# Kernel tuning notes

Measured on AMD Instinct MI355X. Metric: run time of the kernel, lower is better.

Reference implementation:

```python
import jax, jax.numpy as jnp
import numpy as np

EPS = 1e-8

def setup_inputs() -> dict:
    key = jax.random.key(0)
    ks = jax.random.split(key, 4)
    B, N, D = 16, 2048, 1024
    APP = 1024
    x = jax.random.normal(ks[0], (B, N, D), dtype=jnp.float32)
    mask = jax.random.uniform(ks[1], (N, B), dtype=jnp.float32)  # [N, B] per original
    Wp = jax.random.normal(ks[2], (1024, D), dtype=jnp.float32) * 0.02
    bp = jnp.zeros((1024,), dtype=jnp.float32)
    Wv = jax.random.normal(ks[3], (APP, D), dtype=jnp.float32) * 0.02
    bv = jnp.zeros((APP,), dtype=jnp.float32)
    return {"x": x, "mask": mask, "Wp": Wp, "bp": bp, "Wv": Wv, "bv": bv}

def reference(x, mask, Wp, bp, Wv, bv):
    # proj + ReLU: [B,N,1024]
    xp = jax.nn.relu(jnp.einsum('bnd,pd->bnp', x, Wp) + bp)
    # L2-normalize along feature dim (matches xp / (norm + eps))
    xp = xp / (jnp.linalg.norm(xp, axis=2, keepdims=True) + EPS)
    # mask: [N,B] -> [B,N] (transpose+reshape in original yields [B,1,N])
    m = mask.T  # [B, N]
    # att_i = sum_j m_j * <xp_i, xp_j> / sum_j m_j  == <xp_i, sum_j m_j xp_j> / sum_j m_j
    ws = jnp.einsum('bn,bnp->bp', m, xp)                # [B, 1024]
    att = jnp.einsum('bnp,bp->bn', xp, ws) / jnp.sum(m, axis=1, keepdims=True)  # [B, N]
    # value + ReLU: [B,N,APP]
    xv = jax.nn.relu(jnp.einsum('bnd,ad->bna', x, Wv) + bv)
    return att[:, :, None] * xv
```

## Files before the change

kernel.cpp:

```cpp
#include <hip/hip_runtime.h>

#define B_  16
#define N_  2048
#define D_  1024
#define P_  1024
#define M_  (B_*N_)

typedef __attribute__((ext_vector_type(8))) short bf16x8;
typedef __attribute__((ext_vector_type(4))) float f32x4;

__device__ __forceinline__ float bf2f(unsigned short u) {
    union { unsigned int i; float f; } v; v.i = ((unsigned int)u) << 16; return v.f;
}
__device__ __forceinline__ unsigned short f2bf(float f) {
    union { unsigned int i; float f; } v; v.f = f;
    unsigned int i = v.i;
    return (unsigned short)((i + 0x7FFFu + ((i >> 16) & 1u)) >> 16);
}

__device__ __forceinline__ void async_cp16(const void* g, void* s) {
    __builtin_amdgcn_global_load_lds((const __attribute__((address_space(1))) void*)g,
                                     (__attribute__((address_space(3))) void*)s,
                                     16, 0, 0);
}

__global__ void cvt_k(const float* __restrict__ in, unsigned short* __restrict__ out, int n)
{
    for (int i = (blockIdx.x * 256 + threadIdx.x) * 4; i < n; i += gridDim.x * 256 * 4) {
        float4 v = *(const float4*)(in + i);
        union { unsigned short u[4]; unsigned long long ll; } p;
        p.u[0] = f2bf(v.x); p.u[1] = f2bf(v.y); p.u[2] = f2bf(v.z); p.u[3] = f2bf(v.w);
        *(unsigned long long*)(out + i) = p.ll;
    }
}

template<int MODE>
__global__ __launch_bounds__(256) void gemm_bf(const unsigned short* __restrict__ A,
                                               const unsigned short* __restrict__ W,
                                               const float* __restrict__ bias,
                                               const float* __restrict__ att,
                                               void* __restrict__ Cv)
{
    const int K = D_, BK = 32;
    __shared__ unsigned short As[128 * 32];
    __shared__ unsigned short Bs[128 * 32];

    const int wave = threadIdx.x >> 6, lane = threadIdx.x & 63;
    const int wr = wave >> 1, wc = wave & 1;
    const int m0 = blockIdx.y * 128, p0 = blockIdx.x * 128;

    const int srow = wave * 32 + (lane >> 2);
    const int scol = (lane & 3) * 8;
    const unsigned short* ag = A + (size_t)(m0 + srow) * K + scol;
    const unsigned short* bg = W + (size_t)(p0 + srow) * K + scol;
    unsigned short* as = &As[srow * BK + scol];
    unsigned short* bs = &Bs[srow * BK + scol];

    f32x4 acc[4][4];
    #pragma unroll
    for (int i = 0; i < 4; i++)
        #pragma unroll
        for (int j = 0; j < 4; j++) acc[i][j] = (f32x4){0.f,0.f,0.f,0.f};

    const int lr = lane & 15, lq = lane >> 4;
    const unsigned short* Ar = &As[(wr * 64 + lr) * BK + lq * 8];
    const unsigned short* Br = &Bs[(wc * 64 + lr) * BK + lq * 8];

    for (int kb = 0; kb < K; kb += BK) {
        async_cp16(ag + kb,          as);
        async_cp16(ag + 16 * K + kb, as + 16 * BK);
        async_cp16(bg + kb,          bs);
        async_cp16(bg + 16 * K + kb, bs + 16 * BK);
        __syncthreads();
        bf16x8 af[4], bf[4];
        #pragma unroll
        for (int i = 0; i < 4; i++) af[i] = *(const bf16x8*)(Ar + i * 16 * BK);
        #pragma unroll
        for (int j = 0; j < 4; j++) bf[j] = *(const bf16x8*)(Br + j * 16 * BK);
        #pragma unroll
        for (int i = 0; i < 4; i++)
            #pragma unroll
            for (int j = 0; j < 4; j++)
                acc[i][j] = __builtin_amdgcn_mfma_f32_16x16x32_bf16(af[i], bf[j], acc[i][j], 0, 0, 0);
        __syncthreads();
    }

    const int crow0 = m0 + wr * 64 + lq * 4;
    const int ccol0 = p0 + wc * 64 + lr;
    #pragma unroll
    for (int i = 0; i < 4; i++) {
        float attv[4];
        if (MODE == 1) {
            #pragma unroll
            for (int v = 0; v < 4; v++) attv[v] = att[crow0 + i * 16 + v];
        }
        #pragma unroll
        for (int j = 0; j < 4; j++) {
            const int col = ccol0 + j * 16;
            const float bi = bias[col];
            #pragma unroll
            for (int v = 0; v < 4; v++) {
                const int row = crow0 + i * 16 + v;
                float val = fmaxf(acc[i][j][v] + bi, 0.0f);
                if (MODE == 0) ((unsigned short*)Cv)[(size_t)row * P_ + col] = f2bf(val);
                else           ((float*)Cv)[(size_t)row * P_ + col] = val * attv[v];
            }
        }
    }
}

template<int MODE>
__global__ __launch_bounds__(256) void gemm_f32(const float* __restrict__ A,
                                                const float* __restrict__ W,
                                                const float* __restrict__ bias,
                                                const float* __restrict__ att,
                                                void* __restrict__ Cv)
{
    const int K = D_, BK = 32;
    __shared__ float As[128 * 32];
    __shared__ float Bs[128 * 32];

    const int wave = threadIdx.x >> 6, lane = threadIdx.x & 63;
    const int wr = wave >> 1, wc = wave & 1;
    const int m0 = blockIdx.y * 128, p0 = blockIdx.x * 128;

    const int srow = wave * 32 + (lane >> 3);
    const int scol = (lane & 7) * 4;
    const float* ag = A + (size_t)(m0 + srow) * K + scol;
    const float* bg = W + (size_t)(p0 + srow) * K + scol;
    float* as = &As[srow * BK + scol];
    float* bs = &Bs[srow * BK + scol];

    f32x4 acc[4][4];
    #pragma unroll
    for (int i = 0; i < 4; i++)
        #pragma unroll
        for (int j = 0; j < 4; j++) acc[i][j] = (f32x4){0.f,0.f,0.f,0.f};

    const int lr = lane & 15, lq = lane >> 4;
    const float* Ar = &As[(wr * 64 + lr) * BK + lq * 8];
    const float* Br = &Bs[(wc * 64 + lr) * BK + lq * 8];

    for (int kb = 0; kb < K; kb += BK) {
        #pragma unroll
        for (int s = 0; s < 4; s++) {
            async_cp16(ag + (size_t)s * 8 * K + kb, as + s * 8 * BK);
            async_cp16(bg + (size_t)s * 8 * K + kb, bs + s * 8 * BK);
        }
        __syncthreads();
        bf16x8 af[4], bf[4];
        #pragma unroll
        for (int i = 0; i < 4; i++) {
            f32x4 a0 = *(const f32x4*)(Ar + i * 16 * BK);
            f32x4 a1 = *(const f32x4*)(Ar + i * 16 * BK + 4);
            #pragma unroll
            for (int e = 0; e < 4; e++) {
                union { float f; unsigned int u; } c;
                c.f = a0[e]; af[i][e]     = (short)(c.u >> 16);
                c.f = a1[e]; af[i][e + 4] = (short)(c.u >> 16);
            }
        }
        #pragma unroll
        for (int j = 0; j < 4; j++) {
            f32x4 b0 = *(const f32x4*)(Br + j * 16 * BK);
            f32x4 b1 = *(const f32x4*)(Br + j * 16 * BK + 4);
            #pragma unroll
            for (int e = 0; e < 4; e++) {
                union { float f; unsigned int u; } c;
                c.f = b0[e]; bf[j][e]     = (short)(c.u >> 16);
                c.f = b1[e]; bf[j][e + 4] = (short)(c.u >> 16);
            }
        }
        #pragma unroll
        for (int i = 0; i < 4; i++)
            #pragma unroll
            for (int j = 0; j < 4; j++)
                acc[i][j] = __builtin_amdgcn_mfma_f32_16x16x32_bf16(af[i], bf[j], acc[i][j], 0, 0, 0);
        __syncthreads();
    }

    const int crow0 = m0 + wr * 64 + lq * 4;
    const int ccol0 = p0 + wc * 64 + lr;
    #pragma unroll
    for (int i = 0; i < 4; i++) {
        float attv[4];
        if (MODE == 1) {
            #pragma unroll
            for (int v = 0; v < 4; v++) attv[v] = att[crow0 + i * 16 + v];
        }
        #pragma unroll
        for (int j = 0; j < 4; j++) {
            const int col = ccol0 + j * 16;
            const float bi = bias[col];
            #pragma unroll
            for (int v = 0; v < 4; v++) {
                const int row = crow0 + i * 16 + v;
                float val = fmaxf(acc[i][j][v] + bi, 0.0f);
                if (MODE == 0) ((unsigned short*)Cv)[(size_t)row * P_ + col] = f2bf(val);
                else           ((float*)Cv)[(size_t)row * P_ + col] = val * attv[v];
            }
        }
    }
}

__global__ void rownorm_k(const unsigned short* __restrict__ X1,
                          const float* __restrict__ mask,
                          float* __restrict__ inv, float* __restrict__ wgt)
{
    const int r = blockIdx.x * 4 + (threadIdx.x >> 6);
    const int lane = threadIdx.x & 63;
    const unsigned short* row = X1 + (size_t)r * P_;
    bf16x8 u0 = *(const bf16x8*)(row + lane * 8);
    bf16x8 u1 = *(const bf16x8*)(row + 512 + lane * 8);
    float s = 0.f;
    #pragma unroll
    for (int k = 0; k < 8; k++) { float a = bf2f((unsigned short)u0[k]); s += a * a; }
    #pragma unroll
    for (int k = 0; k < 8; k++) { float a = bf2f((unsigned short)u1[k]); s += a * a; }
    #pragma unroll
    for (int off = 32; off > 0; off >>= 1) s += __shfl_down(s, off);
    if (lane == 0) {
        float iv = 1.f / (sqrtf(s) + 1e-8f);
        int b = r >> 11, n = r & (N_ - 1);
        inv[r] = iv;
        wgt[r] = mask[n * B_ + b] * iv;
    }
}

__global__ void msum_k(const float* __restrict__ mask, float* __restrict__ msum)
{
    const int b = blockIdx.x;
    float s = 0.f;
    for (int n = threadIdx.x; n < N_; n += 256) s += mask[n * B_ + b];
    __shared__ float red[256];
    red[threadIdx.x] = s; __syncthreads();
    for (int o = 128; o > 0; o >>= 1) {
        if (threadIdx.x < o) red[threadIdx.x] += red[threadIdx.x + o];
        __syncthreads();
    }
    if (threadIdx.x == 0) msum[b] = red[0];
}

__global__ void colreduce_k(const unsigned short* __restrict__ X1,
                            const float* __restrict__ wgt,
                            float* __restrict__ wsvec)
{
    const int b  = blockIdx.y;
    const int nc = blockIdx.x;
    const int p4 = threadIdx.x * 4;
    float s0 = 0, s1 = 0, s2 = 0, s3 = 0;
    const int rbase = b * N_ + nc * 128;
    for (int n = 0; n < 128; n++) {
        const int r = rbase + n;
        const float w = wgt[r];
        unsigned long long d = *(const unsigned long long*)(X1 + (size_t)r * P_ + p4);
        s0 += w * bf2f((unsigned short)(d));
        s1 += w * bf2f((unsigned short)(d >> 16));
        s2 += w * bf2f((unsigned short)(d >> 32));
        s3 += w * bf2f((unsigned short)(d >> 48));
    }
    float* dst = wsvec + b * P_ + p4;
    atomicAdd(dst + 0, s0); atomicAdd(dst + 1, s1);
    atomicAdd(dst + 2, s2); atomicAdd(dst + 3, s3);
}

__global__ void att_k(const unsigned short* __restrict__ X1,
                      const float* __restrict__ wsvec,
                      const float* __restrict__ inv,
                      const float* __restrict__ msum,
                      float* __restrict__ att)
{
    const int r = blockIdx.x * 4 + (threadIdx.x >> 6);
    const int lane = threadIdx.x & 63;
    const int b = r >> 11;
    const unsigned short* row = X1 + (size_t)r * P_;
    const float* w = wsvec + b * P_;
    bf16x8 u0 = *(const bf16x8*)(row + lane * 8);
    bf16x8 u1 = *(const bf16x8*)(row + 512 + lane * 8);
    float s = 0.f;
    #pragma unroll
    for (int k = 0; k < 8; k++) s += bf2f((unsigned short)u0[k]) * w[lane * 8 + k];
    #pragma unroll
    for (int k = 0; k < 8; k++) s += bf2f((unsigned short)u1[k]) * w[512 + lane * 8 + k];
    #pragma unroll
    for (int off = 32; off > 0; off >>= 1) s += __shfl_down(s, off);
    if (lane == 0) att[r] = s * inv[r] / msum[b];
}

extern "C" void kernel_launch(void* const* d_in, const int* in_sizes, int n_in,
                              void* d_out, int out_size, void* d_ws, size_t ws_size,
                              hipStream_t stream)
{
    const float* x    = (const float*)d_in[0];
    const float* mask = (const float*)d_in[1];
    const float* Wp   = (const float*)d_in[2];
    const float* bp   = (const float*)d_in[3];
    const float* Wv   = (const float*)d_in[4];
    const float* bv   = (const float*)d_in[5];
    float* out = (float*)d_out;

    unsigned short* X1 = (unsigned short*)d_out;

    const size_t xb_bytes = (size_t)M_ * D_ * 2;
    const size_t wb_bytes = (size_t)P_ * D_ * 2;
    const size_t f_bytes  = 3 * (size_t)M_ * 4 + (size_t)B_ * P_ * 4 + 64;
    const bool big_ws = ws_size >= xb_bytes + 2 * wb_bytes + f_bytes;

    char* ws = (char*)d_ws;
    size_t off = 0;
    unsigned short *xb = nullptr, *Wpb = nullptr, *Wvb = nullptr;
    if (big_ws) {
        xb  = (unsigned short*)(ws + off); off += xb_bytes;
        Wpb = (unsigned short*)(ws + off); off += wb_bytes;
        Wvb = (unsigned short*)(ws + off); off += wb_bytes;
    }
    float* inv  = (float*)(ws + off); off += (size_t)M_ * 4;
    float* wgt  = (float*)(ws + off); off += (size_t)M_ * 4;
    float* att  = (float*)(ws + off); off += (size_t)M_ * 4;
    float* wsv  = (float*)(ws + off); off += (size_t)B_ * P_ * 4;
    float* msum = (float*)(ws + off); off += 64;

    hipMemsetAsync(wsv, 0, (size_t)B_ * P_ * 4, stream);

    dim3 g(P_ / 128, M_ / 128);
    if (big_ws) {
        cvt_k<<<2048, 256, 0, stream>>>(x,  xb,  M_ * D_);
        cvt_k<<<256,  256, 0, stream>>>(Wp, Wpb, P_ * D_);
        cvt_k<<<256,  256, 0, stream>>>(Wv, Wvb, P_ * D_);
        gemm_bf<0><<<g, 256, 0, stream>>>(xb, Wpb, bp, nullptr, X1);
    } else {
        gemm_f32<0><<<g, 256, 0, stream>>>(x, Wp, bp, nullptr, X1);
    }
    rownorm_k<<<M_ / 4, 256, 0, stream>>>(X1, mask, inv, wgt);
    msum_k<<<B_, 256, 0, stream>>>(mask, msum);
    colreduce_k<<<dim3(16, B_), 256, 0, stream>>>(X1, wgt, wsv);
    att_k<<<M_ / 4, 256, 0, stream>>>(X1, wsv, inv, msum, att);
    if (big_ws) gemm_bf<1><<<g, 256, 0, stream>>>(xb, Wvb, bv, att, out);
    else        gemm_f32<1><<<g, 256, 0, stream>>>(x, Wv, bv, att, out);
}
```

Measured before the change: 476.6 us.

## Fuse rownorm/colreduce/msum, swizzle LDS, remap GEMM blocks, merge convert kernels

Merges the three fp32-to-bf16 conversion launches into one kernel. Replaces the separate row-norm, mask-sum and column-reduce kernels with a single pass that computes each row's norm and its weighted contribution while the row is already in registers, so X1 is read once less. Adds an XOR swizzle on the bf16 GEMM's LDS tile to reduce bank conflicts, and remaps the 1D grid into groups of eight M-tiles that share a weight tile for better L2 reuse. The fused reduction uses fewer blocks (256), which may lower parallelism for that stage.

```diff
diff --git a/kernel.cpp b/kernel.cpp
--- a/kernel.cpp
+++ b/kernel.cpp
@@ -24,13 +24,29 @@
                                      16, 0, 0);
 }
 
-__global__ void cvt_k(const float* __restrict__ in, unsigned short* __restrict__ out, int n)
-{
-    for (int i = (blockIdx.x * 256 + threadIdx.x) * 4; i < n; i += gridDim.x * 256 * 4) {
-        float4 v = *(const float4*)(in + i);
+__global__ void cvt_all_k(const float* __restrict__ x,  unsigned short* __restrict__ xb,
+                          const float* __restrict__ Wp, unsigned short* __restrict__ Wpb,
+                          const float* __restrict__ Wv, unsigned short* __restrict__ Wvb)
+{
+    const int stride = gridDim.x * 256 * 4;
+    const int base = (blockIdx.x * 256 + threadIdx.x) * 4;
+    for (int i = base; i < M_ * D_; i += stride) {
+        float4 v = *(const float4*)(x + i);
         union { unsigned short u[4]; unsigned long long ll; } p;
-        p.u[0] = f2bf(v.x); p.u[1] = f2bf(v.y); p.u[2] = f2bf(v.z); p.u[3] = f2bf(v.w);
-        *(unsigned long long*)(out + i) = p.ll;
+        p.u[0]=f2bf(v.x); p.u[1]=f2bf(v.y); p.u[2]=f2bf(v.z); p.u[3]=f2bf(v.w);
+        *(unsigned long long*)(xb + i) = p.ll;
+    }
+    for (int i = base; i < P_ * D_; i += stride) {
+        float4 v = *(const float4*)(Wp + i);
+        union { unsigned short u[4]; unsigned long long ll; } p;
+        p.u[0]=f2bf(v.x); p.u[1]=f2bf(v.y); p.u[2]=f2bf(v.z); p.u[3]=f2bf(v.w);
+        *(unsigned long long*)(Wpb + i) = p.ll;
+    }
+    for (int i = base; i < P_ * D_; i += stride) {
+        float4 v = *(const float4*)(Wv + i);
+        union { unsigned short u[4]; unsigned long long ll; } p;
+        p.u[0]=f2bf(v.x); p.u[1]=f2bf(v.y); p.u[2]=f2bf(v.z); p.u[3]=f2bf(v.w);
+        *(unsigned long long*)(Wvb + i) = p.ll;
     }
 }
 
@@ -45,16 +61,22 @@
     __shared__ unsigned short As[128 * 32];
     __shared__ unsigned short Bs[128 * 32];
 
+    const int id = blockIdx.x;
+    const int bx = (id >> 3) & 7;
+    const int by = ((id >> 6) << 3) | (id & 7);
+    const int m0 = by * 128, p0 = bx * 128;
+
     const int wave = threadIdx.x >> 6, lane = threadIdx.x & 63;
     const int wr = wave >> 1, wc = wave & 1;
-    const int m0 = blockIdx.y * 128, p0 = blockIdx.x * 128;
-
-    const int srow = wave * 32 + (lane >> 2);
-    const int scol = (lane & 3) * 8;
-    const unsigned short* ag = A + (size_t)(m0 + srow) * K + scol;
-    const unsigned short* bg = W + (size_t)(p0 + srow) * K + scol;
-    unsigned short* as = &As[srow * BK + scol];
-    unsigned short* bs = &Bs[srow * BK + scol];
+
+    const int srow  = wave * 32 + (lane >> 2);
+    const int schk  = (lane & 3) ^ ((lane >> 3) & 3);
+    const int scolg = schk * 8;
+    const int scold = (lane & 3) * 8;
+    const unsigned short* ag = A + (size_t)(m0 + srow) * K + scolg;
+    const unsigned short* bg = W + (size_t)(p0 + srow) * K + scolg;
+    unsigned short* as = &As[srow * BK + scold];
+    unsigned short* bs = &Bs[srow * BK + scold];
 
     f32x4 acc[4][4];
     #pragma unroll
@@ -63,8 +85,9 @@
         for (int j = 0; j < 4; j++) acc[i][j] = (f32x4){0.f,0.f,0.f,0.f};
 
     const int lr = lane & 15, lq = lane >> 4;
-    const unsigned short* Ar = &As[(wr * 64 + lr) * BK + lq * 8];
-    const unsigned short* Br = &Bs[(wc * 64 + lr) * BK + lq * 8];
+    const int swz = (lr >> 1) & 3;
+    const unsigned short* Ar = &As[(wr * 64 + lr) * BK + ((lq ^ swz) * 8)];
+    const unsigned short* Br = &Bs[(wc * 64 + lr) * BK + ((lq ^ swz) * 8)];
 
     for (int kb = 0; kb < K; kb += BK) {
         async_cp16(ag + kb,          as);
@@ -119,28 +142,26 @@
     const int K = D_, BK = 32;
     __shared__ float As[128 * 32];
     __shared__ float Bs[128 * 32];
-
+    const int id = blockIdx.x;
+    const int bx = (id >> 3) & 7;
+    const int by = ((id >> 6) << 3) | (id & 7);
+    const int m0 = by * 128, p0 = bx * 128;
     const int wave = threadIdx.x >> 6, lane = threadIdx.x & 63;
     const int wr = wave >> 1, wc = wave & 1;
-    const int m0 = blockIdx.y * 128, p0 = blockIdx.x * 128;
-
     const int srow = wave * 32 + (lane >> 3);
     const int scol = (lane & 7) * 4;
     const float* ag = A + (size_t)(m0 + srow) * K + scol;
     const float* bg = W + (size_t)(p0 + srow) * K + scol;
     float* as = &As[srow * BK + scol];
     float* bs = &Bs[srow * BK + scol];
-
     f32x4 acc[4][4];
     #pragma unroll
     for (int i = 0; i < 4; i++)
         #pragma unroll
         for (int j = 0; j < 4; j++) acc[i][j] = (f32x4){0.f,0.f,0.f,0.f};
-
     const int lr = lane & 15, lq = lane >> 4;
     const float* Ar = &As[(wr * 64 + lr) * BK + lq * 8];
     const float* Br = &Bs[(wc * 64 + lr) * BK + lq * 8];
-
     for (int kb = 0; kb < K; kb += BK) {
         #pragma unroll
         for (int s = 0; s < 4; s++) {
@@ -178,7 +199,6 @@
                 acc[i][j] = __builtin_amdgcn_mfma_f32_16x16x32_bf16(af[i], bf[j], acc[i][j], 0, 0, 0);
         __syncthreads();
     }
-
     const int crow0 = m0 + wr * 64 + lq * 4;
     const int ccol0 = p0 + wc * 64 + lr;
     #pragma unroll
@@ -203,65 +223,54 @@
     }
 }
 
-__global__ void rownorm_k(const unsigned short* __restrict__ X1,
-                          const float* __restrict__ mask,
-                          float* __restrict__ inv, float* __restrict__ wgt)
-{
-    const int r = blockIdx.x * 4 + (threadIdx.x >> 6);
-    const int lane = threadIdx.x & 63;
-    const unsigned short* row = X1 + (size_t)r * P_;
-    bf16x8 u0 = *(const bf16x8*)(row + lane * 8);
-    bf16x8 u1 = *(const bf16x8*)(row + 512 + lane * 8);
-    float s = 0.f;
-    #pragma unroll
-    for (int k = 0; k < 8; k++) { float a = bf2f((unsigned short)u0[k]); s += a * a; }
-    #pragma unroll
-    for (int k = 0; k < 8; k++) { float a = bf2f((unsigned short)u1[k]); s += a * a; }
-    #pragma unroll
-    for (int off = 32; off > 0; off >>= 1) s += __shfl_down(s, off);
-    if (lane == 0) {
-        float iv = 1.f / (sqrtf(s) + 1e-8f);
-        int b = r >> 11, n = r & (N_ - 1);
-        inv[r] = iv;
-        wgt[r] = mask[n * B_ + b] * iv;
-    }
-}
-
-__global__ void msum_k(const float* __restrict__ mask, float* __restrict__ msum)
-{
-    const int b = blockIdx.x;
-    float s = 0.f;
-    for (int n = threadIdx.x; n < N_; n += 256) s += mask[n * B_ + b];
-    __shared__ float red[256];
-    red[threadIdx.x] = s; __syncthreads();
-    for (int o = 128; o > 0; o >>= 1) {
-        if (threadIdx.x < o) red[threadIdx.x] += red[threadIdx.x + o];
-        __syncthreads();
-    }
-    if (threadIdx.x == 0) msum[b] = red[0];
-}
-
-__global__ void colreduce_k(const unsigned short* __restrict__ X1,
-                            const float* __restrict__ wgt,
-                            float* __restrict__ wsvec)
-{
-    const int b  = blockIdx.y;
-    const int nc = blockIdx.x;
-    const int p4 = threadIdx.x * 4;
-    float s0 = 0, s1 = 0, s2 = 0, s3 = 0;
-    const int rbase = b * N_ + nc * 128;
-    for (int n = 0; n < 128; n++) {
-        const int r = rbase + n;
-        const float w = wgt[r];
-        unsigned long long d = *(const unsigned long long*)(X1 + (size_t)r * P_ + p4);
-        s0 += w * bf2f((unsigned short)(d));
-        s1 += w * bf2f((unsigned short)(d >> 16));
-        s2 += w * bf2f((unsigned short)(d >> 32));
-        s3 += w * bf2f((unsigned short)(d >> 48));
-    }
-    float* dst = wsvec + b * P_ + p4;
-    atomicAdd(dst + 0, s0); atomicAdd(dst + 1, s1);
-    atomicAdd(dst + 2, s2); atomicAdd(dst + 3, s3);
+__global__ __launch_bounds__(256) void fused_nc_k(const unsigned short* __restrict__ X1,
+                                                  const float* __restrict__ mask,
+                                                  float* __restrict__ inv,
+                                                  float* __restrict__ wsv,
+                                                  float* __restrict__ msum)
+{
+    __shared__ float accw[4][1024];
+    __shared__ float mred[4];
+    const int b = blockIdx.y, nc = blockIdx.x;
+    const int wave = threadIdx.x >> 6, lane = threadIdx.x & 63;
+    float acc[16];
+    #pragma unroll
+    for (int e = 0; e < 16; e++) acc[e] = 0.f;
+    float msub = 0.f;
+    const int rbase = b * N_ + nc * 128 + wave * 32;
+    const int nbase = nc * 128 + wave * 32;
+    for (int t = 0; t < 32; t++) {
+        const int r = rbase + t;
+        const unsigned short* row = X1 + (size_t)r * P_;
+        bf16x8 u0 = *(const bf16x8*)(row + lane * 16);
+        bf16x8 u1 = *(const bf16x8*)(row + lane * 16 + 8);
+        float v[16], s = 0.f;
+        #pragma unroll
+        for (int e = 0; e < 8; e++) { v[e] = bf2f((unsigned short)u0[e]); s += v[e]*v[e]; }
+        #pragma unroll
+        for (int e = 0; e < 8; e++) { v[8+e] = bf2f((unsigned short)u1[e]); s += v[8+e]*v[8+e]; }
+        #pragma unroll
+        for (int off = 32; off > 0; off >>= 1) s += __shfl_down(s, off);
+        s = __shfl(s, 0);
+        const float iv = 1.f / (sqrtf(s) + 1e-8f);
+        const float mk = mask[(nbase + t) * B_ + b];
+        if (lane == 0) { inv[r] = iv; msub += mk; }
+        const float w = mk * iv;
+        #pragma unroll
+        for (int e = 0; e < 16; e++) acc[e] += w * v[e];
+    }
+    #pragma unroll
+    for (int e = 0; e < 16; e++) accw[wave][e * 64 + lane] = acc[e];
+    if (lane == 0) mred[wave] = msub;
+    __syncthreads();
+    #pragma unroll
+    for (int q = 0; q < 4; q++) {
+        const int p = threadIdx.x * 4 + q;
+        const int col = (p & 63) * 16 + (p >> 6);
+        float ssum = accw[0][p] + accw[1][p] + accw[2][p] + accw[3][p];
+        atomicAdd(&wsv[b * P_ + col], ssum);
+    }
+    if (threadIdx.x == 0) atomicAdd(&msum[b], mred[0] + mred[1] + mred[2] + mred[3]);
 }
 
 __global__ void att_k(const unsigned short* __restrict__ X1,
@@ -303,7 +312,7 @@
 
     const size_t xb_bytes = (size_t)M_ * D_ * 2;
     const size_t wb_bytes = (size_t)P_ * D_ * 2;
-    const size_t f_bytes  = 3 * (size_t)M_ * 4 + (size_t)B_ * P_ * 4 + 64;
+    const size_t f_bytes  = 2 * (size_t)M_ * 4 + (size_t)B_ * P_ * 4 + 64;
     const bool big_ws = ws_size >= xb_bytes + 2 * wb_bytes + f_bytes;
 
     char* ws = (char*)d_ws;
@@ -315,26 +324,21 @@
         Wvb = (unsigned short*)(ws + off); off += wb_bytes;
     }
     float* inv  = (float*)(ws + off); off += (size_t)M_ * 4;
-    float* wgt  = (float*)(ws + off); off += (size_t)M_ * 4;
     float* att  = (float*)(ws + off); off += (size_t)M_ * 4;
     float* wsv  = (float*)(ws + off); off += (size_t)B_ * P_ * 4;
     float* msum = (float*)(ws + off); off += 64;
 
-    hipMemsetAsync(wsv, 0, (size_t)B_ * P_ * 4, stream);
-
-    dim3 g(P_ / 128, M_ / 128);
+    hipMemsetAsync(wsv, 0, (size_t)B_ * P_ * 4 + 64, stream);
+
+    const int gblocks = (P_ / 128) * (M_ / 128);
     if (big_ws) {
-        cvt_k<<<2048, 256, 0, stream>>>(x,  xb,  M_ * D_);
-        cvt_k<<<256,  256, 0, stream>>>(Wp, Wpb, P_ * D_);
-        cvt_k<<<256,  256, 0, stream>>>(Wv, Wvb, P_ * D_);
-        gemm_bf<0><<<g, 256, 0, stream>>>(xb, Wpb, bp, nullptr, X1);
+        cvt_all_k<<<2048, 256, 0, stream>>>(x, xb, Wp, Wpb, Wv, Wvb);
+        gemm_bf<0><<<gblocks, 256, 0, stream>>>(xb, Wpb, bp, nullptr, X1);
     } else {
-        gemm_f32<0><<<g, 256, 0, stream>>>(x, Wp, bp, nullptr, X1);
-    }
-    rownorm_k<<<M_ / 4, 256, 0, stream>>>(X1, mask, inv, wgt);
-    msum_k<<<B_, 256, 0, stream>>>(mask, msum);
-    colreduce_k<<<dim3(16, B_), 256, 0, stream>>>(X1, wgt, wsv);
+        gemm_f32<0><<<gblocks, 256, 0, stream>>>(x, Wp, bp, nullptr, X1);
+    }
+    fused_nc_k<<<dim3(16, B_), 256, 0, stream>>>(X1, mask, inv, wsv, msum);
     att_k<<<M_ / 4, 256, 0, stream>>>(X1, wsv, inv, msum, att);
-    if (big_ws) gemm_bf<1><<<g, 256, 0, stream>>>(xb, Wvb, bv, att, out);
-    else        gemm_f32<1><<<g, 256, 0, stream>>>(x, Wv, bv, att, out);
-}
+    if (big_ws) gemm_bf<1><<<gblocks, 256, 0, stream>>>(xb, Wvb, bv, att, out);
+    else        gemm_f32<1><<<gblocks, 256, 0, stream>>>(x, Wv, bv, att, out);
+}
```

Result: faster. 434.3 us (-8.9%).
